# Optimization experiments

Hardware: AMD Instinct MI355X
Metric: run time of the kernel (lower is better)

Reference implementation:

```python
import jax, jax.numpy as jnp
import numpy as np

B, P, H, N, D, K = 1024, 1024, 4096, 32, 512, 128


def setup_inputs() -> dict:
    key = jax.random.key(0)
    k1, k2, k3, k4, k5 = jax.random.split(key, 5)
    return {
        "proximal_input": jax.random.normal(k1, (B, P), dtype=jnp.float32),
        "distal_input": jax.random.normal(k2, (B, D), dtype=jnp.float32),
        "W": jax.random.normal(k3, (H, P), dtype=jnp.float32) / np.sqrt(P),
        "b": jax.random.normal(k4, (H,), dtype=jnp.float32) / np.sqrt(P),
        "distal": jax.random.normal(k5, (H, N, D), dtype=jnp.float32),
        "k": K,
    }


def reference(proximal_input, distal_input, W, b, distal, k):
    # proximal path: standard linear -> (B, H)
    proximal_output = proximal_input @ W.T + b
    # per-hidden-unit dendrite projections -> (H, B, N)
    distal_output = jnp.einsum('bd,hnd->hbn', distal_input, distal)
    # pick dominant dendrite by absolute value, keep its signed value
    abs_max_idx = jnp.argmax(jnp.abs(distal_output), axis=-1)          # (H, B)
    distal_max = jnp.take_along_axis(
        distal_output, abs_max_idx[..., None], axis=-1)[..., 0].T      # (B, H)
    # sigmoid gate modulates proximal activations
    result = proximal_output * jax.nn.sigmoid(distal_max)              # (B, H)
    # keep only top-k per row (scatter-built 0/1 mask, as in the original)
    _, top_idxs = jax.lax.top_k(result, k)                             # (B, k)
    rows = jnp.arange(result.shape[0])[:, None]
    mask = jnp.zeros_like(result).at[rows, top_idxs].set(1.0)
    return result * mask
```

## Files before the change

kernel.cpp:

```cpp
#include <hip/hip_runtime.h>
#include <cstdint>
#include <cmath>

#define Bsz  1024
#define Pdim 1024
#define Hdim 4096
#define Ndim 32
#define Ddim 512
#define Ktop 128

typedef _Float16 f16x8  __attribute__((ext_vector_type(8)));
typedef float    f32x16 __attribute__((ext_vector_type(16)));

#define GLDS(gsrc, ldst)                                                        \
  __builtin_amdgcn_global_load_lds(                                             \
      (const __attribute__((address_space(1))) unsigned int*)(gsrc),            \
      (__attribute__((address_space(3))) unsigned int*)(ldst), 16, 0, 0)

#define WS_NEEDED 270532608ull

__global__ __launch_bounds__(256) void convert_img(
    const float* __restrict__ src, char* __restrict__ dst, int kcbits)
{
  const int gid  = blockIdx.x * 256 + threadIdx.x;
  const int row  = gid >> kcbits;
  const int e    = (gid & ((1 << kcbits) - 1)) * 8;
  const int Krow = 8 << kcbits;
  float4 v0 = *(const float4*)(src + (size_t)row * Krow + e);
  float4 v1 = *(const float4*)(src + (size_t)row * Krow + e + 4);
  const int tile = row >> 7, r = row & 127, ks = e >> 5, k = e & 31;
  char* base = dst + (size_t)(tile * (Krow >> 5) + ks) * 16384;
  const int off = ((r >> 5) * 2 + (k >> 4)) * 1024
                + ((r & 31) + 32 * ((k >> 3) & 1)) * 16;
  const float f[8] = {v0.x, v0.y, v0.z, v0.w, v1.x, v1.y, v1.z, v1.w};
  f16x8 hi, lo;
#pragma unroll
  for (int j = 0; j < 8; j++) {
    const _Float16 h = (_Float16)f[j];
    hi[j] = h;
    lo[j] = (_Float16)((f[j] - (float)h) * 256.f);
  }
  *(f16x8*)(base + off)        = hi;
  *(f16x8*)(base + 8192 + off) = lo;
}

#define VMWAIT(N)                                            \
  asm volatile("s_waitcnt vmcnt(" #N ")" ::: "memory");      \
  __builtin_amdgcn_sched_barrier(0)

#define LOADB(H, BH, BL)                                                        \
  { const char* sB = Bwave + (size_t)((H) >> 1) * 16384 + ((H) & 1) * 1024 + lane16; \
    BH[0] = *(const f16x8*)(sB);                                                \
    BH[1] = *(const f16x8*)(sB + 2048);                                         \
    BL[0] = *(const f16x8*)(sB + 8192);                                         \
    BL[1] = *(const f16x8*)(sB + 8192 + 2048);                                  \
    __builtin_amdgcn_sched_barrier(0); }

#define STAGE_A(H)                                                              \
  { char* dA = priv + ((H) & 3) * 4096;                                         \
    const char* sA = Awave + (size_t)((H) >> 1) * 16384 + ((H) & 1) * 1024 + lane16; \
    GLDS(sA,                dA);                                                \
    GLDS(sA + 2048,         dA + 1024);                                         \
    GLDS(sA + 8192,         dA + 2048);                                         \
    GLDS(sA + 8192 + 2048,  dA + 3072); }

#define COMPUTE(H, BH, BL)                                                      \
  { const char* buf = priv + ((H) & 3) * 4096 + lane16;                         \
    f16x8 ah[2], al[2];                                                         \
    ah[0] = *(const f16x8*)(buf);                                               \
    ah[1] = *(const f16x8*)(buf + 1024);                                        \
    al[0] = *(const f16x8*)(buf + 2048);                                        \
    al[1] = *(const f16x8*)(buf + 3072);                                        \
    __builtin_amdgcn_s_setprio(1);                                              \
    _Pragma("unroll")                                                           \
    for (int ni = 0; ni < 2; ni++)                                              \
      _Pragma("unroll")                                                         \
      for (int mi = 0; mi < 2; mi++) {                                          \
        acc[mi][ni]  = __builtin_amdgcn_mfma_f32_32x32x16_f16(ah[mi], BH[ni], acc[mi][ni],  0, 0, 0); \
        accx[mi][ni] = __builtin_amdgcn_mfma_f32_32x32x16_f16(ah[mi], BL[ni], accx[mi][ni], 0, 0, 0); \
        accx[mi][ni] = __builtin_amdgcn_mfma_f32_32x32x16_f16(al[mi], BH[ni], accx[mi][ni], 0, 0, 0); \
      }                                                                         \
    __builtin_amdgcn_s_setprio(0); }

#define PIPE_LOOP(NH)                                                           \
  f16x8 bh0[2], bl0[2], bh1[2], bl1[2];                                         \
  LOADB(0, bh0, bl0);                                                           \
  STAGE_A(0); STAGE_A(1);                                                       \
  int h = 0;                                                                    \
  for (; h + 3 < (NH); h += 2) {                                                \
    LOADB(h + 1, bh1, bl1); STAGE_A(h + 2); VMWAIT(12); COMPUTE(h, bh0, bl0);   \
    LOADB(h + 2, bh0, bl0); STAGE_A(h + 3); VMWAIT(12); COMPUTE(h + 1, bh1, bl1); \
  }                                                                             \
  LOADB(h + 1, bh1, bl1); VMWAIT(8); COMPUTE(h, bh0, bl0);                      \
  VMWAIT(0); COMPUTE(h + 1, bh1, bl1);

__global__ __launch_bounds__(256, 2) void proximal_mfma(
    const char* __restrict__ Aw, const char* __restrict__ Bw,
    const float* __restrict__ bias, float* __restrict__ out)
{
  __shared__ __align__(16) char lds[4][4][4096];
  const int t = threadIdx.x, lane = t & 63, wv = t >> 6;
  const int lane16 = lane * 16;
  const int hi32 = lane >> 5, c31 = lane & 31;
  const int wr = wv >> 1, wc = wv & 1;
  char* priv = &lds[wv][0][0];

  const int blk = blockIdx.x;
  const int xcd = blk & 7, q = blk >> 3;
  const int htile = xcd * 4 + (q >> 3);
  const int btile = q & 7;
  const int h0 = htile * 128, b0 = btile * 128;

  f32x16 acc[2][2], accx[2][2];
#pragma unroll
  for (int mi = 0; mi < 2; mi++)
#pragma unroll
    for (int ni = 0; ni < 2; ni++) {
      acc[mi][ni]  = (f32x16)(0.f);
      accx[mi][ni] = (f32x16)(0.f);
    }

  const char* Awave = Aw + (size_t)(htile * 32) * 16384 + wr * 4096;
  const char* Bwave = Bw + (size_t)(btile * 32) * 16384 + wc * 4096;

  PIPE_LOOP(64)

#pragma unroll
  for (int mi = 0; mi < 2; ++mi)
#pragma unroll
    for (int ni = 0; ni < 2; ++ni) {
      const int bcol = b0 + wc * 64 + ni * 32 + c31;
#pragma unroll
      for (int qq = 0; qq < 4; ++qq) {
        const int hb = h0 + wr * 64 + mi * 32 + qq * 8 + hi32 * 4;
        const float4 bb = *(const float4*)(bias + hb);
        float4 o;
        o.x = acc[mi][ni][4*qq+0] + accx[mi][ni][4*qq+0] * 0.00390625f + bb.x;
        o.y = acc[mi][ni][4*qq+1] + accx[mi][ni][4*qq+1] * 0.00390625f + bb.y;
        o.z = acc[mi][ni][4*qq+2] + accx[mi][ni][4*qq+2] * 0.00390625f + bb.z;
        o.w = acc[mi][ni][4*qq+3] + accx[mi][ni][4*qq+3] * 0.00390625f + bb.w;
        *(float4*)(out + (size_t)bcol * Hdim + hb) = o;
      }
    }
}

__global__ __launch_bounds__(256, 2) void distal_mfma(
    const char* __restrict__ Aw, const char* __restrict__ Bw,
    float* __restrict__ out)
{
  __shared__ __align__(16) char lds[4][4][4096];
  const int t = threadIdx.x, lane = t & 63, wv = t >> 6;
  const int lane16 = lane * 16;
  const int hi32 = lane >> 5, c31 = lane & 31;
  const int wr = wv >> 1, wc = wv & 1;
  char* priv = &lds[wv][0][0];

  const int blk = blockIdx.x;
  const int xcd = blk & 7, q = blk >> 3;
  const int ntile = xcd * 128 + (q >> 3);
  const int btile = q & 7;

  f32x16 acc[2][2], accx[2][2];
#pragma unroll
  for (int mi = 0; mi < 2; mi++)
#pragma unroll
    for (int ni = 0; ni < 2; ni++) {
      acc[mi][ni]  = (f32x16)(0.f);
      accx[mi][ni] = (f32x16)(0.f);
    }

  const char* Awave = Aw + (size_t)(ntile * 16) * 16384 + wr * 4096;
  const char* Bwave = Bw + (size_t)(btile * 16) * 16384 + wc * 4096;

  PIPE_LOOP(32)

#pragma unroll
  for (int mi = 0; mi < 2; ++mi)
#pragma unroll
    for (int ni = 0; ni < 2; ++ni) {
      float bestA = -1.f, bestV = 0.f;
      int   bestN = 999;
#pragma unroll
      for (int reg = 0; reg < 16; ++reg) {
        const float v = acc[mi][ni][reg] + accx[mi][ni][reg] * 0.00390625f;
        const float a = fabsf(v);
        const int   n = (reg & 3) + 8 * (reg >> 2) + 4 * hi32;
        if (a > bestA) { bestA = a; bestV = v; bestN = n; }
      }
      {
        const float oa = __shfl_xor(bestA, 32, 64);
        const float ov = __shfl_xor(bestV, 32, 64);
        const int   on = __shfl_xor(bestN, 32, 64);
        if (oa > bestA || (oa == bestA && on < bestN)) {
          bestA = oa; bestV = ov; bestN = on;
        }
      }
      if (hi32 == 0) {
        const int bcol = btile * 128 + wc * 64 + ni * 32 + c31;
        const int h    = ntile * 4 + wr * 2 + mi;
        const float gate = 1.f / (1.f + expf(-bestV));
        out[(size_t)bcol * Hdim + h] *= gate;
      }
    }
}

__global__ __launch_bounds__(256) void proximal_gemm(
    const float* __restrict__ pin, const float* __restrict__ W,
    const float* __restrict__ bias, float* __restrict__ out)
{
  __shared__ float Blds[32 * 256];
  __shared__ float Alds[32 * 32];
  const int t  = threadIdx.x;
  const int l  = t & 63;
  const int wv = t >> 6;
  const int ell   = blockIdx.x;
  const int xcd   = ell & 7;
  const int q     = ell >> 3;
  const int htile = xcd * 2 + (q >> 5);
  const int btile = q & 31;
  const int h0 = htile * 256, b0 = btile * 32;

  float acc[8][4];
#pragma unroll
  for (int i = 0; i < 8; i++)
    for (int j = 0; j < 4; j++) acc[i][j] = 0.f;

  const float* wrow = W + (size_t)(h0 + t) * Pdim;
  const int ab = t >> 3, ak = (t & 7) * 4;
  const float* arow = pin + (size_t)(b0 + ab) * Pdim + ak;

  for (int kt = 0; kt < Pdim / 32; ++kt) {
    const int p0 = kt * 32;
    float wbuf[32];
#pragma unroll
    for (int f = 0; f < 8; f++) {
      float4 v = *(const float4*)(wrow + p0 + f * 4);
      wbuf[f * 4 + 0] = v.x; wbuf[f * 4 + 1] = v.y;
      wbuf[f * 4 + 2] = v.z; wbuf[f * 4 + 3] = v.w;
    }
    float4 av = *(const float4*)(arow + p0);
    __syncthreads();
#pragma unroll
    for (int f = 0; f < 32; f++) Blds[f * 256 + t] = wbuf[f];
    Alds[(ak + 0) * 32 + ab] = av.x;
    Alds[(ak + 1) * 32 + ab] = av.y;
    Alds[(ak + 2) * 32 + ab] = av.z;
    Alds[(ak + 3) * 32 + ab] = av.w;
    __syncthreads();
#pragma unroll
    for (int k = 0; k < 32; k++) {
      float4 bv  = *(const float4*)&Blds[k * 256 + 4 * l];
      float4 alo = *(const float4*)&Alds[k * 32 + 8 * wv];
      float4 ahi = *(const float4*)&Alds[k * 32 + 8 * wv + 4];
      float a0[8] = {alo.x, alo.y, alo.z, alo.w, ahi.x, ahi.y, ahi.z, ahi.w};
#pragma unroll
      for (int i = 0; i < 8; i++) {
        acc[i][0] += a0[i] * bv.x;
        acc[i][1] += a0[i] * bv.y;
        acc[i][2] += a0[i] * bv.z;
        acc[i][3] += a0[i] * bv.w;
      }
    }
  }
  float4 bb = *(const float4*)(bias + h0 + 4 * l);
#pragma unroll
  for (int i = 0; i < 8; i++) {
    float4 o;
    o.x = acc[i][0] + bb.x;
    o.y = acc[i][1] + bb.y;
    o.z = acc[i][2] + bb.z;
    o.w = acc[i][3] + bb.w;
    *(float4*)(out + (size_t)(b0 + 8 * wv + i) * Hdim + h0 + 4 * l) = o;
  }
}

__global__ __launch_bounds__(256) void distal_gate_fb(
    const float* __restrict__ din, const float* __restrict__ distal,
    float* __restrict__ out)
{
  __shared__ float Blds[32 * 256];
  __shared__ float Alds[32 * 32];
  const int t  = threadIdx.x;
  const int l  = t & 63;
  const int wv = t >> 6;
  const int ell   = blockIdx.x;
  const int xcd   = ell & 7;
  const int q     = ell >> 3;
  const int htile = xcd * 64 + (q >> 5);
  const int btile = q & 31;
  const int n0 = htile * 256, b0 = btile * 32;

  float acc[8][4];
#pragma unroll
  for (int i = 0; i < 8; i++)
    for (int j = 0; j < 4; j++) acc[i][j] = 0.f;

  const float* brow = distal + (size_t)(n0 + t) * Ddim;
  const int ab = t >> 3, ak = (t & 7) * 4;
  const float* arow = din + (size_t)(b0 + ab) * Ddim + ak;

  for (int kt = 0; kt < Ddim / 32; ++kt) {
    const int d0 = kt * 32;
    float wbuf[32];
#pragma unroll
    for (int f = 0; f < 8; f++) {
      float4 v = *(const float4*)(brow + d0 + f * 4);
      wbuf[f * 4 + 0] = v.x; wbuf[f * 4 + 1] = v.y;
      wbuf[f * 4 + 2] = v.z; wbuf[f * 4 + 3] = v.w;
    }
    float4 av = *(const float4*)(arow + d0);
    __syncthreads();
#pragma unroll
    for (int f = 0; f < 32; f++) Blds[f * 256 + t] = wbuf[f];
    Alds[(ak + 0) * 32 + ab] = av.x;
    Alds[(ak + 1) * 32 + ab] = av.y;
    Alds[(ak + 2) * 32 + ab] = av.z;
    Alds[(ak + 3) * 32 + ab] = av.w;
    __syncthreads();
#pragma unroll
    for (int k = 0; k < 32; k++) {
      float4 bv  = *(const float4*)&Blds[k * 256 + 4 * l];
      float4 alo = *(const float4*)&Alds[k * 32 + 8 * wv];
      float4 ahi = *(const float4*)&Alds[k * 32 + 8 * wv + 4];
      float a0[8] = {alo.x, alo.y, alo.z, alo.w, ahi.x, ahi.y, ahi.z, ahi.w};
#pragma unroll
      for (int i = 0; i < 8; i++) {
        acc[i][0] += a0[i] * bv.x;
        acc[i][1] += a0[i] * bv.y;
        acc[i][2] += a0[i] * bv.z;
        acc[i][3] += a0[i] * bv.w;
      }
    }
  }
  const int i0  = l & 7;
  const int grp = l >> 3;
  float v = 0.f;
#pragma unroll
  for (int bi = 0; bi < 8; bi++) {
    float bav = fabsf(acc[bi][0]);
    float bv_ = acc[bi][0];
    int   bn  = 4 * i0;
#pragma unroll
    for (int j = 1; j < 4; j++) {
      float av2 = fabsf(acc[bi][j]);
      if (av2 > bav) { bav = av2; bv_ = acc[bi][j]; bn = 4 * i0 + j; }
    }
#pragma unroll
    for (int m = 1; m < 8; m <<= 1) {
      float oav = __shfl_xor(bav, m, 64);
      float ov  = __shfl_xor(bv_, m, 64);
      int   on  = __shfl_xor(bn,  m, 64);
      if (oav > bav || (oav == bav && on < bn)) { bav = oav; bv_ = ov; bn = on; }
    }
    if (bi == i0) v = bv_;
  }
  const float gate = 1.f / (1.f + expf(-v));
  const size_t idx = (size_t)(b0 + 8 * wv + i0) * Hdim + (size_t)htile * 8 + grp;
  out[idx] *= gate;
}

__device__ __forceinline__ unsigned keyf(float f) {
  unsigned u = __float_as_uint(f);
  return (u & 0x80000000u) ? ~u : (u | 0x80000000u);
}

__global__ __launch_bounds__(256) void topk_mask(float* __restrict__ out)
{
  __shared__ float vals[Hdim];
  __shared__ unsigned hist[256];
  __shared__ unsigned sc[4];
  __shared__ unsigned s_prefix, s_kk;
  const int t = threadIdx.x;
  float* row = out + (size_t)blockIdx.x * Hdim;

#pragma unroll
  for (int qq = 0; qq < 4; qq++) {
    float4 v = *(const float4*)(row + qq * 1024 + t * 4);
    *(float4*)&vals[qq * 1024 + t * 4] = v;
  }
  if (t == 0) { s_prefix = 0u; s_kk = Ktop; }
  __syncthreads();

  for (int shift = 24; shift >= 0; shift -= 8) {
    hist[t] = 0u;
    __syncthreads();
    const unsigned prefix = s_prefix;
    const unsigned maskhi = (shift == 24) ? 0u : (0xFFFFFFFFu << (shift + 8));
    for (int c = 0; c < 16; c++) {
      unsigned u = keyf(vals[c * 256 + t]);
      if ((u & maskhi) == prefix)
        atomicAdd(&hist[(u >> shift) & 255u], 1u);
    }
    __syncthreads();
    if (t == 0) {
      unsigned kk = s_kk, cum = 0;
      int bin = 255;
      for (; bin > 0; --bin) {
        unsigned c = hist[bin];
        if (cum + c >= kk) break;
        cum += c;
      }
      s_kk = kk - cum;
      s_prefix = prefix | ((unsigned)bin << shift);
    }
    __syncthreads();
  }
  const unsigned T  = s_prefix;
  const unsigned kk = s_kk;

  const int lane = t & 63, w = t >> 6;
  unsigned running = 0;
  for (int c = 0; c < 16; c++) {
    const int h = c * 256 + t;
    const float v = vals[h];
    const unsigned u = keyf(v);
    const bool tie = (u == T);
    unsigned long long m = __ballot(tie);
    unsigned lpfx = (unsigned)__popcll(m & ((1ull << lane) - 1ull));
    if (lane == 0) sc[w] = (unsigned)__popcll(m);
    __syncthreads();
    unsigned off = 0;
#pragma unroll
    for (int ww = 0; ww < 4; ww++) if (ww < w) off += sc[ww];
    const unsigned rank = running + off + lpfx;
    row[h] = (u > T) ? v : ((tie && rank < kk) ? v : 0.f);
    const unsigned tot = sc[0] + sc[1] + sc[2] + sc[3];
    __syncthreads();
    running += tot;
  }
}

extern "C" void kernel_launch(void* const* d_in, const int* in_sizes, int n_in,
                              void* d_out, int out_size, void* d_ws, size_t ws_size,
                              hipStream_t stream)
{
  (void)in_sizes; (void)n_in; (void)out_size;
  const float* pin  = (const float*)d_in[0];
  const float* dinp = (const float*)d_in[1];
  const float* W    = (const float*)d_in[2];
  const float* bias = (const float*)d_in[3];
  const float* dst  = (const float*)d_in[4];
  float* out = (float*)d_out;

  if (ws_size >= WS_NEEDED) {
    char* ws = (char*)d_ws;
    hipLaunchKernelGGL(convert_img,   dim3(2048),  dim3(256), 0, stream, W,   ws,             7);
    hipLaunchKernelGGL(convert_img,   dim3(512),   dim3(256), 0, stream, pin, ws + 16777216,  7);
    hipLaunchKernelGGL(proximal_mfma, dim3(256),   dim3(256), 0, stream, ws, ws + 16777216, bias, out);
    hipLaunchKernelGGL(convert_img,   dim3(32768), dim3(256), 0, stream, dst,  ws,             6);
    hipLaunchKernelGGL(convert_img,   dim3(256),   dim3(256), 0, stream, dinp, ws + 268435456, 6);
    hipLaunchKernelGGL(distal_mfma,   dim3(8192),  dim3(256), 0, stream, ws, ws + 268435456, out);
  } else {
    hipLaunchKernelGGL(proximal_gemm, dim3(512),   dim3(256), 0, stream, pin, W, bias, out);
    hipLaunchKernelGGL(distal_gate_fb, dim3(16384), dim3(256), 0, stream, dinp, dst, out);
  }

  hipLaunchKernelGGL(topk_mask, dim3(Bsz), dim3(256), 0, stream, out);
}
```

Before: 696.0 us.

## Share A-tile LDS staging across waves with workgroup barriers

Each wave previously staged its own private copy of the A tile into LDS, so the two waves sharing a row loaded the same A data twice. Now the four waves cooperatively load one shared A buffer (two chunks each) and read their rows from it, halving A global traffic and LDS footprint. In exchange, a workgroup barrier is needed before each compute step, which couples the waves and may reduce latency hiding; the vmcnt wait counts are adjusted to match.

```diff
diff --git a/kernel.cpp b/kernel.cpp
--- a/kernel.cpp
+++ b/kernel.cpp
@@ -48,6 +48,10 @@
   asm volatile("s_waitcnt vmcnt(" #N ")" ::: "memory");      \
   __builtin_amdgcn_sched_barrier(0)
 
+#define BARRIER()                                            \
+  __builtin_amdgcn_s_barrier();                              \
+  __builtin_amdgcn_sched_barrier(0)
+
 #define LOADB(H, BH, BL)                                                        \
   { const char* sB = Bwave + (size_t)((H) >> 1) * 16384 + ((H) & 1) * 1024 + lane16; \
     BH[0] = *(const f16x8*)(sB);                                                \
@@ -57,20 +61,23 @@
     __builtin_amdgcn_sched_barrier(0); }
 
 #define STAGE_A(H)                                                              \
-  { char* dA = priv + ((H) & 3) * 4096;                                         \
-    const char* sA = Awave + (size_t)((H) >> 1) * 16384 + ((H) & 1) * 1024 + lane16; \
-    GLDS(sA,                dA);                                                \
-    GLDS(sA + 2048,         dA + 1024);                                         \
-    GLDS(sA + 8192,         dA + 2048);                                         \
-    GLDS(sA + 8192 + 2048,  dA + 3072); }
+  { char* buf = &lds[(H) & 3][0];                                               \
+    const char* Ai = Abase + (size_t)((H) >> 1) * 16384;                        \
+    const int kk = (H) & 1;                                                     \
+    _Pragma("unroll")                                                           \
+    for (int j = 0; j < 2; j++) {                                               \
+      const int ch = wv * 2 + j;                                                \
+      const char* src = Ai + (ch >> 2) * 8192 + (2 * (ch & 3) + kk) * 1024 + lane16; \
+      GLDS(src, buf + ch * 1024);                                               \
+    } }
 
 #define COMPUTE(H, BH, BL)                                                      \
-  { const char* buf = priv + ((H) & 3) * 4096 + lane16;                         \
+  { const char* buf = &lds[(H) & 3][0] + lane16;                                \
     f16x8 ah[2], al[2];                                                         \
-    ah[0] = *(const f16x8*)(buf);                                               \
-    ah[1] = *(const f16x8*)(buf + 1024);                                        \
-    al[0] = *(const f16x8*)(buf + 2048);                                        \
-    al[1] = *(const f16x8*)(buf + 3072);                                        \
+    ah[0] = *(const f16x8*)(buf + (2 * wr + 0) * 1024);                         \
+    ah[1] = *(const f16x8*)(buf + (2 * wr + 1) * 1024);                         \
+    al[0] = *(const f16x8*)(buf + 4096 + (2 * wr + 0) * 1024);                  \
+    al[1] = *(const f16x8*)(buf + 4096 + (2 * wr + 1) * 1024);                  \
     __builtin_amdgcn_s_setprio(1);                                              \
     _Pragma("unroll")                                                           \
     for (int ni = 0; ni < 2; ni++)                                              \
@@ -88,22 +95,23 @@
   STAGE_A(0); STAGE_A(1);                                                       \
   int h = 0;                                                                    \
   for (; h + 3 < (NH); h += 2) {                                                \
-    LOADB(h + 1, bh1, bl1); STAGE_A(h + 2); VMWAIT(12); COMPUTE(h, bh0, bl0);   \
-    LOADB(h + 2, bh0, bl0); STAGE_A(h + 3); VMWAIT(12); COMPUTE(h + 1, bh1, bl1); \
+    LOADB(h + 1, bh1, bl1); STAGE_A(h + 2); VMWAIT(8); BARRIER();               \
+    COMPUTE(h, bh0, bl0);                                                       \
+    LOADB(h + 2, bh0, bl0); STAGE_A(h + 3); VMWAIT(8); BARRIER();               \
+    COMPUTE(h + 1, bh1, bl1);                                                   \
   }                                                                             \
-  LOADB(h + 1, bh1, bl1); VMWAIT(8); COMPUTE(h, bh0, bl0);                      \
-  VMWAIT(0); COMPUTE(h + 1, bh1, bl1);
+  LOADB(h + 1, bh1, bl1); VMWAIT(6); BARRIER(); COMPUTE(h, bh0, bl0);           \
+  VMWAIT(0); BARRIER(); COMPUTE(h + 1, bh1, bl1);
 
 __global__ __launch_bounds__(256, 2) void proximal_mfma(
     const char* __restrict__ Aw, const char* __restrict__ Bw,
     const float* __restrict__ bias, float* __restrict__ out)
 {
-  __shared__ __align__(16) char lds[4][4][4096];
+  __shared__ __align__(16) char lds[4][8192];
   const int t = threadIdx.x, lane = t & 63, wv = t >> 6;
   const int lane16 = lane * 16;
   const int hi32 = lane >> 5, c31 = lane & 31;
   const int wr = wv >> 1, wc = wv & 1;
-  char* priv = &lds[wv][0][0];
 
   const int blk = blockIdx.x;
   const int xcd = blk & 7, q = blk >> 3;
@@ -120,7 +128,7 @@
       accx[mi][ni] = (f32x16)(0.f);
     }
 
-  const char* Awave = Aw + (size_t)(htile * 32) * 16384 + wr * 4096;
+  const char* Abase = Aw + (size_t)(htile * 32) * 16384;
   const char* Bwave = Bw + (size_t)(btile * 32) * 16384 + wc * 4096;
 
   PIPE_LOOP(64)
@@ -148,12 +156,11 @@
     const char* __restrict__ Aw, const char* __restrict__ Bw,
     float* __restrict__ out)
 {
-  __shared__ __align__(16) char lds[4][4][4096];
+  __shared__ __align__(16) char lds[4][8192];
   const int t = threadIdx.x, lane = t & 63, wv = t >> 6;
   const int lane16 = lane * 16;
   const int hi32 = lane >> 5, c31 = lane & 31;
   const int wr = wv >> 1, wc = wv & 1;
-  char* priv = &lds[wv][0][0];
 
   const int blk = blockIdx.x;
   const int xcd = blk & 7, q = blk >> 3;
@@ -169,7 +176,7 @@
       accx[mi][ni] = (f32x16)(0.f);
     }
 
-  const char* Awave = Aw + (size_t)(ntile * 16) * 16384 + wr * 4096;
+  const char* Abase = Aw + (size_t)(ntile * 16) * 16384;
   const char* Bwave = Bw + (size_t)(btile * 16) * 16384 + wc * 4096;
 
   PIPE_LOOP(32)
```

Result: faster. 664.0 us (-4.6%).
